# Optimization experiments

Measured on AMD Instinct MI355X. Metric: run time of the kernel, lower is better.

## Reference

```python
import jax, jax.numpy as jnp
import numpy as np

B, S, D, H = 4, 1024, 1024, 16
DK = D // H
NEG = -1e9


def setup_inputs() -> dict:
    key = jax.random.key(0)
    ks = jax.random.split(key, 14)
    sc = 1.0 / np.sqrt(D)
    inp = {
        "query": jax.random.normal(ks[0], (B, S, D), jnp.float32),
        "key": jax.random.normal(ks[1], (B, S, D), jnp.float32),
        "value": jax.random.normal(ks[2], (B, S, D), jnp.float32),
        "mask": jax.random.randint(ks[3], (B, S, S), 0, 2, jnp.int32),
        "group_prob": jax.random.uniform(ks[4], (B, S, S), jnp.float32),
        "Wq": jax.random.normal(ks[5], (D, D), jnp.float32) * sc,
        "bq": jnp.zeros((D,), jnp.float32),
        "Wk": jax.random.normal(ks[6], (D, D), jnp.float32) * sc,
        "bk": jnp.zeros((D,), jnp.float32),
        "Wv": jax.random.normal(ks[7], (D, D), jnp.float32) * sc,
        "bv": jnp.zeros((D,), jnp.float32),
        "Wo": jax.random.normal(ks[8], (D, D), jnp.float32) * sc,
        "bo": jnp.zeros((D,), jnp.float32),
    }
    return inp


def reference(query, key, value, mask, group_prob, Wq, bq, Wk, bk, Wv, bv, Wo, bo):
    # QKV projections, split heads: [B,S,D] -> [B,H,S,DK]
    def proj(x, W, b):
        return (x @ W.T + b).reshape(B, S, H, DK).transpose(0, 2, 1, 3)

    q = proj(query, Wq, bq)
    k = proj(key, Wk, bk)
    v = proj(value, Wv, bv)

    scores = jnp.einsum("bhqd,bhkd->bhqk", q, k) / jnp.sqrt(jnp.float32(DK))

    # group_prob branch: allowed where mask OR diagonal is nonzero
    diag = jnp.eye(S, dtype=jnp.int32)
    allowed = (mask[:, None, :, :] | diag[None, None, :, :]) != 0  # [B,1,S,S]
    scores = jnp.where(allowed, scores, NEG)

    p_attn = jax.nn.softmax(scores, axis=-1)
    p_attn = p_attn * group_prob[:, None, :, :]  # post-softmax group reweighting

    x = jnp.einsum("bhqk,bhkd->bhqd", p_attn, v)
    x = x.transpose(0, 2, 1, 3).reshape(B, S, D)
    return x @ Wo.T + bo
```

## Files before the change

kernel.cpp:

```cpp
#include <hip/hip_runtime.h>
#include <hip/hip_bf16.h>


#define AS1q __attribute__((address_space(1)))
#define AS3q __attribute__((address_space(3)))

typedef __attribute__((ext_vector_type(8))) __bf16 bf16x8;
typedef __attribute__((ext_vector_type(4))) float f32x4;
typedef __attribute__((ext_vector_type(8))) unsigned short u16x8;

#define GSTR 40

__device__ __forceinline__ void gload_lds16(const void* g, void* l) {
  __builtin_amdgcn_global_load_lds((const AS1q void*)g, (AS3q void*)l, 16, 0, 0);
}
__device__ __forceinline__ bf16x8 lds_read8(const unsigned short* p) {
  bf16x8 r;
  __builtin_memcpy(&r, __builtin_assume_aligned(p, 16), 16);
  return r;
}
__device__ __forceinline__ void lds_write8(unsigned short* p, const void* v) {
  __builtin_memcpy(__builtin_assume_aligned(p, 16), v, 16);
}
__device__ __forceinline__ u16x8 cvt8h(const float4 a, const float4 b) {
  const float fv[8] = {a.x, a.y, a.z, a.w, b.x, b.y, b.z, b.w};
  union { u16x8 v; __bf16 e[8]; } hh;
#pragma unroll
  for (int i = 0; i < 8; ++i) hh.e[i] = (__bf16)fv[i];
  return hh.v;
}
__device__ __forceinline__ void cvt8hl(const float4 a, const float4 b, u16x8* hi, u16x8* lo) {
  const float fv[8] = {a.x, a.y, a.z, a.w, b.x, b.y, b.z, b.w};
  union { u16x8 v; __bf16 e[8]; } hh, ll;
#pragma unroll
  for (int i = 0; i < 8; ++i) {
    const __bf16 h = (__bf16)fv[i];
    hh.e[i] = h;
    ll.e[i] = (__bf16)(fv[i] - (float)h);
  }
  *hi = hh.v; *lo = ll.v;
}
__device__ __forceinline__ unsigned short bfbits(float f) {
  const __bf16 h = (__bf16)f;
  unsigned short u; __builtin_memcpy(&u, &h, 2); return u;
}

__global__ __launch_bounds__(256) void k_prep(
    const int* __restrict__ Mask, const float* __restrict__ Gp, float* __restrict__ G2)
{
  const size_t f = (size_t)blockIdx.x * 256 + threadIdx.x;
  const size_t e = f << 2;
  const int k0 = (int)(e & 1023), q = (int)((e >> 10) & 1023);
  const int4 m4 = *(const int4*)(Mask + e);
  const float4 g4 = *(const float4*)(Gp + e);
  float4 r;
  r.x = (m4.x | (q == k0 + 0)) ? g4.x : -1.f;
  r.y = (m4.y | (q == k0 + 1)) ? g4.y : -1.f;
  r.z = (m4.z | (q == k0 + 2)) ? g4.z : -1.f;
  r.w = (m4.w | (q == k0 + 3)) ? g4.w : -1.f;
  *(float4*)(G2 + e) = r;
}

__global__ __launch_bounds__(256) void k_gemm_qkv(
    const float* __restrict__ X0, const float* __restrict__ X1, const float* __restrict__ X2,
    const float* __restrict__ W0, const float* __restrict__ W1, const float* __restrict__ W2,
    const float* __restrict__ B0, const float* __restrict__ B1, const float* __restrict__ B2,
    unsigned short* __restrict__ O0, unsigned short* __restrict__ O1,
    unsigned short* __restrict__ O2)
{
  const int z = blockIdx.z;
  const float* X = (z == 0) ? X0 : (z == 1) ? X1 : X2;
  const float* W = (z == 0) ? W0 : (z == 1) ? W1 : W2;
  const float* Bi = (z == 0) ? B0 : (z == 1) ? B1 : B2;
  unsigned short* O = (z == 0) ? O0 : (z == 1) ? O1 : O2;

  const int bid = blockIdx.x;
  const int swz = (bid & 7) * 64 + (bid >> 3);
  const int n0 = (swz & 15) * 64, m0 = (swz >> 4) * 128;

  __shared__ alignas(16) unsigned short Ah[128 * GSTR];
  __shared__ alignas(16) unsigned short Bh[64 * GSTR];
  const int tid = threadIdx.x, l = tid & 63, w = tid >> 6;
  const int wr = w >> 1, wc = w & 1;

  f32x4 acc[4][2];
#pragma unroll
  for (int i = 0; i < 4; ++i)
#pragma unroll
    for (int j = 0; j < 2; ++j) acc[i][j] = (f32x4){0.f, 0.f, 0.f, 0.f};

  const int arow = tid >> 1, ac0 = (tid & 1) * 16;
  const int brow = tid >> 2, bc0 = (tid & 3) * 8;
  const float* xsrc = X + (size_t)(m0 + arow) * 1024 + ac0;
  const float* wsrc = W + (size_t)(n0 + brow) * 1024 + bc0;

  float4 fx[4], fw[2];
#pragma unroll
  for (int i = 0; i < 4; ++i) fx[i] = *(const float4*)(xsrc + i * 4);
#pragma unroll
  for (int i = 0; i < 2; ++i) fw[i] = *(const float4*)(wsrc + i * 4);

  for (int kt = 0; kt < 32; ++kt) {
    u16x8 xh[2], wh1;
    xh[0] = cvt8h(fx[0], fx[1]);
    xh[1] = cvt8h(fx[2], fx[3]);
    wh1 = cvt8h(fw[0], fw[1]);
    if (kt < 31) {
      const float* nx = xsrc + (kt + 1) * 32;
      const float* nw = wsrc + (kt + 1) * 32;
#pragma unroll
      for (int i = 0; i < 4; ++i) fx[i] = *(const float4*)(nx + i * 4);
#pragma unroll
      for (int i = 0; i < 2; ++i) fw[i] = *(const float4*)(nw + i * 4);
    }
    __syncthreads();
    lds_write8(&Ah[arow * GSTR + ac0], &xh[0]);
    lds_write8(&Ah[arow * GSTR + ac0 + 8], &xh[1]);
    lds_write8(&Bh[brow * GSTR + bc0], &wh1);
    __syncthreads();

    bf16x8 ah[4], bh[2];
#pragma unroll
    for (int mf = 0; mf < 4; ++mf) {
      const int r = wr * 64 + mf * 16 + (l & 15);
      ah[mf] = lds_read8(&Ah[r * GSTR + (l >> 4) * 8]);
    }
#pragma unroll
    for (int nf = 0; nf < 2; ++nf) {
      const int r = wc * 32 + nf * 16 + (l & 15);
      bh[nf] = lds_read8(&Bh[r * GSTR + (l >> 4) * 8]);
    }
#pragma unroll
    for (int mf = 0; mf < 4; ++mf)
#pragma unroll
      for (int nf = 0; nf < 2; ++nf)
        acc[mf][nf] = __builtin_amdgcn_mfma_f32_16x16x32_bf16(ah[mf], bh[nf], acc[mf][nf], 0, 0, 0);
  }

#pragma unroll
  for (int nf = 0; nf < 2; ++nf) {
    const int col = n0 + wc * 32 + nf * 16 + (l & 15);
    const float bias = Bi[col];
#pragma unroll
    for (int mf = 0; mf < 4; ++mf) {
      const int rbase = m0 + wr * 64 + mf * 16 + (l >> 4) * 4;
#pragma unroll
      for (int j = 0; j < 4; ++j)
        O[(size_t)(rbase + j) * 1024 + col] = bfbits(acc[mf][nf][j] + bias);
    }
  }
}

__global__ __launch_bounds__(256) void k_gemm_out(
    const unsigned short* __restrict__ X, const float* __restrict__ W,
    const float* __restrict__ Bi, float* __restrict__ Out)
{
  const int bid = blockIdx.x;
  const int swz = (bid & 7) * 128 + (bid >> 3);
  const int n0 = (swz & 15) * 64, m0 = (swz >> 4) * 64;

  __shared__ alignas(16) unsigned short Ah[64 * GSTR];
  __shared__ alignas(16) unsigned short Bh[64 * GSTR], Bl[64 * GSTR];
  const int tid = threadIdx.x, l = tid & 63, w = tid >> 6;
  const int wr = w >> 1, wc = w & 1;

  f32x4 acc[2][2];
#pragma unroll
  for (int i = 0; i < 2; ++i)
#pragma unroll
    for (int j = 0; j < 2; ++j) acc[i][j] = (f32x4){0.f, 0.f, 0.f, 0.f};

  const int srow = tid >> 2, sc0 = (tid & 3) * 8;
  const unsigned short* xsrc = X + (size_t)(m0 + srow) * 1024 + sc0;
  const float* wsrc = W + (size_t)(n0 + srow) * 1024 + sc0;

  u16x8 xcur = *(const u16x8*)xsrc;
  float4 fw[2];
#pragma unroll
  for (int i = 0; i < 2; ++i) fw[i] = *(const float4*)(wsrc + i * 4);

  for (int kt = 0; kt < 32; ++kt) {
    const u16x8 xstage = xcur;
    u16x8 wh1, wl1;
    cvt8hl(fw[0], fw[1], &wh1, &wl1);
    if (kt < 31) {
      xcur = *(const u16x8*)(xsrc + (kt + 1) * 32);
      const float* nw = wsrc + (kt + 1) * 32;
#pragma unroll
      for (int i = 0; i < 2; ++i) fw[i] = *(const float4*)(nw + i * 4);
    }
    __syncthreads();
    lds_write8(&Ah[srow * GSTR + sc0], &xstage);
    lds_write8(&Bh[srow * GSTR + sc0], &wh1);
    lds_write8(&Bl[srow * GSTR + sc0], &wl1);
    __syncthreads();

    bf16x8 ah[2], bh[2], bl[2];
#pragma unroll
    for (int mf = 0; mf < 2; ++mf) {
      const int r = wr * 32 + mf * 16 + (l & 15);
      ah[mf] = lds_read8(&Ah[r * GSTR + (l >> 4) * 8]);
    }
#pragma unroll
    for (int nf = 0; nf < 2; ++nf) {
      const int r = wc * 32 + nf * 16 + (l & 15);
      bh[nf] = lds_read8(&Bh[r * GSTR + (l >> 4) * 8]);
      bl[nf] = lds_read8(&Bl[r * GSTR + (l >> 4) * 8]);
    }
#pragma unroll
    for (int mf = 0; mf < 2; ++mf)
#pragma unroll
      for (int nf = 0; nf < 2; ++nf) {
        acc[mf][nf] = __builtin_amdgcn_mfma_f32_16x16x32_bf16(ah[mf], bh[nf], acc[mf][nf], 0, 0, 0);
        acc[mf][nf] = __builtin_amdgcn_mfma_f32_16x16x32_bf16(ah[mf], bl[nf], acc[mf][nf], 0, 0, 0);
      }
  }

#pragma unroll
  for (int nf = 0; nf < 2; ++nf) {
    const int col = n0 + wc * 32 + nf * 16 + (l & 15);
    const float bias = Bi[col];
#pragma unroll
    for (int mf = 0; mf < 2; ++mf) {
      const int rbase = m0 + wr * 32 + mf * 16 + (l >> 4) * 4;
#pragma unroll
      for (int j = 0; j < 4; ++j)
        Out[(size_t)(rbase + j) * 1024 + col] = acc[mf][nf][j] + bias;
    }
  }
}

__global__ __launch_bounds__(256) void k_attn(
    const unsigned short* Qh, const unsigned short* __restrict__ Kb,
    const unsigned short* __restrict__ Vb,
    const float* __restrict__ G2, unsigned short* Xo)
{
  const int i = blockIdx.x;
  const int xc = i & 7, kk_ = i >> 3;
  const int h = kk_ & 15, g = kk_ >> 4;
  const int qb = g * 8 + xc;
  const int qt = qb >> 2, b = qb & 3;

  __shared__ alignas(16) unsigned short Kh[2][64 * 64];
  __shared__ alignas(16) unsigned short Vh[64 * 64];
  __shared__ alignas(16) unsigned short Ph[64 * 64];
  const int tid = threadIdx.x, l = tid & 63, w = tid >> 6;

  const unsigned short* kb_ = Kb + (size_t)b * 1048576 + h * 64;
  const unsigned short* vb_ = Vb + (size_t)b * 1048576 + h * 64;

  bf16x8 aq[2];
  {
    const int qrow = qt * 64 + w * 16 + (l & 15);
    const unsigned short* qp_ = Qh + ((size_t)(b * 1024 + qrow)) * 1024 + h * 64;
    aq[0] = lds_read8(qp_ + (l >> 4) * 8);
    aq[1] = lds_read8(qp_ + 32 + (l >> 4) * 8);
  }

  f32x4 accO[4];
#pragma unroll
  for (int nf = 0; nf < 4; ++nf) accO[nf] = (f32x4){0.f, 0.f, 0.f, 0.f};
  float zacc[4] = {0.f, 0.f, 0.f, 0.f};

  const int qloc0 = w * 16 + (l >> 4) * 4;
  const int qg0 = qt * 64 + qloc0;
  const int mcol = l & 15;

  const float* grow[4];
#pragma unroll
  for (int j = 0; j < 4; ++j)
    grow[j] = G2 + (((size_t)(b * 1024 + qg0 + j)) << 10) + mcol;

  const int srcg8 = ((l & 7) ^ (l >> 3)) * 8;
  const int rowl = l >> 3;
  const int kb4 = (tid & 15) * 4, db4 = (tid >> 4) * 4;
  union U4 { unsigned int u[2]; unsigned short s[4]; };
  U4 vr[4];

#pragma unroll
  for (int I = 0; I < 2; ++I)
    gload_lds16(kb_ + (size_t)(I * 32 + w * 8 + rowl) * 1024 + srcg8,
                &Kh[0][I * 2048 + w * 512]);
#pragma unroll
  for (int ii = 0; ii < 4; ++ii)
    __builtin_memcpy(&vr[ii], vb_ + (size_t)(kb4 + ii) * 1024 + db4, 8);

  float gcur[4][4], gnext[4][4];
#pragma unroll
  for (int nf = 0; nf < 4; ++nf)
#pragma unroll
    for (int j = 0; j < 4; ++j) gcur[nf][j] = grow[j][nf * 16];

  int buf = 0;
  for (int kt = 0; kt < 16; ++kt) {
    __syncthreads();

#pragma unroll
    for (int ii = 0; ii < 4; ++ii) {
      const int d = db4 + ii;
      union { unsigned short s[4]; unsigned long long v; } pk;
#pragma unroll
      for (int u = 0; u < 4; ++u) pk.s[u] = vr[u].s[ii];
      const int c = kb4 ^ ((d & 7) << 3);
      __builtin_memcpy(__builtin_assume_aligned(&Vh[d * 64 + c], 8), &pk.v, 8);
    }
    __syncthreads();

    if (kt < 15) {
#pragma unroll
      for (int I = 0; I < 2; ++I)
        gload_lds16(kb_ + (size_t)((kt + 1) * 64 + I * 32 + w * 8 + rowl) * 1024 + srcg8,
                    &Kh[buf ^ 1][I * 2048 + w * 512]);
#pragma unroll
      for (int ii = 0; ii < 4; ++ii)
        __builtin_memcpy(&vr[ii], vb_ + (size_t)((kt + 1) * 64 + kb4 + ii) * 1024 + db4, 8);
#pragma unroll
      for (int nf = 0; nf < 4; ++nf)
#pragma unroll
        for (int j = 0; j < 4; ++j) gnext[nf][j] = grow[j][(kt + 1) * 64 + nf * 16];
    }

#pragma unroll
    for (int nf = 0; nf < 4; ++nf) {
      f32x4 sacc = (f32x4){0.f, 0.f, 0.f, 0.f};
      const int kr = nf * 16 + (l & 15);
#pragma unroll
      for (int ks = 0; ks < 2; ++ks) {
        const int c = (ks * 32 + (l >> 4) * 8) ^ ((kr & 7) << 3);
        sacc = __builtin_amdgcn_mfma_f32_16x16x32_bf16(aq[ks], lds_read8(&Kh[buf][kr * 64 + c]), sacc, 0, 0, 0);
      }
#pragma unroll
      for (int j = 0; j < 4; ++j) {
        const float g2 = gcur[nf][j];
        const float e = (g2 >= 0.f) ? exp2f(fmaf(sacc[j], 0.18033688f, -17.31234049f)) : 0.f;
        zacc[j] += e;
        const int qloc = qloc0 + j;
        Ph[qloc * 64 + ((nf * 16 + mcol) ^ ((qloc & 7) << 3))] = bfbits(e * g2);
      }
    }
    bf16x8 pah[2];
    {
      const int ar = w * 16 + (l & 15);
#pragma unroll
      for (int ks = 0; ks < 2; ++ks) {
        const int c = (ks * 32 + (l >> 4) * 8) ^ ((ar & 7) << 3);
        pah[ks] = lds_read8(&Ph[ar * 64 + c]);
      }
    }
#pragma unroll
    for (int nf = 0; nf < 4; ++nf) {
      const int dr = nf * 16 + (l & 15);
#pragma unroll
      for (int ks = 0; ks < 2; ++ks) {
        const int c = (ks * 32 + (l >> 4) * 8) ^ ((dr & 7) << 3);
        accO[nf] = __builtin_amdgcn_mfma_f32_16x16x32_bf16(pah[ks], lds_read8(&Vh[dr * 64 + c]), accO[nf], 0, 0, 0);
      }
    }
    buf ^= 1;
#pragma unroll
    for (int nf = 0; nf < 4; ++nf)
#pragma unroll
      for (int j = 0; j < 4; ++j) gcur[nf][j] = gnext[nf][j];
  }

#pragma unroll
  for (int j = 0; j < 4; ++j) {
#pragma unroll
    for (int off = 1; off < 16; off <<= 1) zacc[j] += __shfl_xor(zacc[j], off, 64);
  }
  float rz[4];
#pragma unroll
  for (int j = 0; j < 4; ++j) rz[j] = 1.f / zacc[j];

#pragma unroll
  for (int nf = 0; nf < 4; ++nf) {
    const int d = nf * 16 + (l & 15);
#pragma unroll
    for (int j = 0; j < 4; ++j) {
      const int qg = qg0 + j;
      Xo[((size_t)(b * 1024 + qg)) * 1024 + h * 64 + d] = bfbits(accO[nf][j] * rz[j]);
    }
  }
}

extern "C" void kernel_launch(void* const* d_in, const int* in_sizes, int n_in,
                              void* d_out, int out_size, void* d_ws, size_t ws_size,
                              hipStream_t stream) {
  const float* query = (const float*)d_in[0];
  const float* key_in = (const float*)d_in[1];
  const float* value = (const float*)d_in[2];
  const int* mask = (const int*)d_in[3];
  const float* gp = (const float*)d_in[4];
  const float* Wq = (const float*)d_in[5];
  const float* bq = (const float*)d_in[6];
  const float* Wk = (const float*)d_in[7];
  const float* bk = (const float*)d_in[8];
  const float* Wv = (const float*)d_in[9];
  const float* bv = (const float*)d_in[10];
  const float* Wo = (const float*)d_in[11];
  const float* bo = (const float*)d_in[12];
  float* out = (float*)d_out;

  unsigned short* kp = (unsigned short*)d_ws;
  unsigned short* vp = kp + 4194304;
  unsigned short* qp = vp + 4194304;
  unsigned short* xo = qp;
  float* g2 = (float*)(qp + 4194304);

  hipLaunchKernelGGL(k_prep, dim3(4096), dim3(256), 0, stream, mask, gp, g2);
  hipLaunchKernelGGL(k_gemm_qkv, dim3(512, 1, 3), dim3(256), 0, stream,
                     query, key_in, value, Wq, Wk, Wv, bq, bk, bv, qp, kp, vp);
  hipLaunchKernelGGL(k_attn, dim3(1024), dim3(256), 0, stream,
                     qp, kp, vp, g2, xo);
  hipLaunchKernelGGL(k_gemm_out, dim3(1024), dim3(256), 0, stream,
                     xo, Wo, bo, out);
}
```

Baseline: 186.3 us.

## Pre-convert QKV weights to bf16 and double-buffer LDS in QKV GEMM

Adds a separate kernel that converts Wq/Wk/Wv to bf16 once per call, so the QKV GEMM reads half the weight bytes and skips per-tile weight conversion. The QKV GEMM now uses double-buffered LDS tiles with a two-stage register prefetch, which cuts the barriers per k-step from two to one. The cost is an extra launch, extra workspace traffic for the bf16 weight copies, and twice the LDS per block.

```diff
diff --git a/kernel.cpp b/kernel.cpp
--- a/kernel.cpp
+++ b/kernel.cpp
@@ -45,7 +45,7 @@
   unsigned short u; __builtin_memcpy(&u, &h, 2); return u;
 }
 
-__global__ __launch_bounds__(256) void k_prep(
+__global__ __launch_bounds__(256) void k_prep_g2(
     const int* __restrict__ Mask, const float* __restrict__ Gp, float* __restrict__ G2)
 {
   const size_t f = (size_t)blockIdx.x * 256 + threadIdx.x;
@@ -61,16 +61,32 @@
   *(float4*)(G2 + e) = r;
 }
 
+__global__ __launch_bounds__(256) void k_prep_w(
+    const float* __restrict__ Wq, const float* __restrict__ Wk,
+    const float* __restrict__ Wv,
+    unsigned short* __restrict__ Qw, unsigned short* __restrict__ Kw,
+    unsigned short* __restrict__ Vw)
+{
+  const int z = blockIdx.z;
+  const size_t e = ((size_t)blockIdx.x * 256 + threadIdx.x) * 8;
+  const float* S = (z == 0) ? Wq : (z == 1) ? Wk : Wv;
+  unsigned short* D = (z == 0) ? Qw : (z == 1) ? Kw : Vw;
+  const float4 a = *(const float4*)(S + e);
+  const float4 b = *(const float4*)(S + e + 4);
+  *(u16x8*)(D + e) = cvt8h(a, b);
+}
+
 __global__ __launch_bounds__(256) void k_gemm_qkv(
     const float* __restrict__ X0, const float* __restrict__ X1, const float* __restrict__ X2,
-    const float* __restrict__ W0, const float* __restrict__ W1, const float* __restrict__ W2,
+    const unsigned short* __restrict__ W0, const unsigned short* __restrict__ W1,
+    const unsigned short* __restrict__ W2,
     const float* __restrict__ B0, const float* __restrict__ B1, const float* __restrict__ B2,
     unsigned short* __restrict__ O0, unsigned short* __restrict__ O1,
     unsigned short* __restrict__ O2)
 {
   const int z = blockIdx.z;
   const float* X = (z == 0) ? X0 : (z == 1) ? X1 : X2;
-  const float* W = (z == 0) ? W0 : (z == 1) ? W1 : W2;
+  const unsigned short* W = (z == 0) ? W0 : (z == 1) ? W1 : W2;
   const float* Bi = (z == 0) ? B0 : (z == 1) ? B1 : B2;
   unsigned short* O = (z == 0) ? O0 : (z == 1) ? O1 : O2;
 
@@ -78,8 +94,8 @@
   const int swz = (bid & 7) * 64 + (bid >> 3);
   const int n0 = (swz & 15) * 64, m0 = (swz >> 4) * 128;
 
-  __shared__ alignas(16) unsigned short Ah[128 * GSTR];
-  __shared__ alignas(16) unsigned short Bh[64 * GSTR];
+  __shared__ alignas(16) unsigned short Ah[2][128 * GSTR];
+  __shared__ alignas(16) unsigned short Bh[2][64 * GSTR];
   const int tid = threadIdx.x, l = tid & 63, w = tid >> 6;
   const int wr = w >> 1, wc = w & 1;
 
@@ -92,49 +108,55 @@
   const int arow = tid >> 1, ac0 = (tid & 1) * 16;
   const int brow = tid >> 2, bc0 = (tid & 3) * 8;
   const float* xsrc = X + (size_t)(m0 + arow) * 1024 + ac0;
-  const float* wsrc = W + (size_t)(n0 + brow) * 1024 + bc0;
-
-  float4 fx[4], fw[2];
+  const unsigned short* wsrc = W + (size_t)(n0 + brow) * 1024 + bc0;
+
+  float4 fx[4];
+  u16x8 bx;
 #pragma unroll
   for (int i = 0; i < 4; ++i) fx[i] = *(const float4*)(xsrc + i * 4);
-#pragma unroll
-  for (int i = 0; i < 2; ++i) fw[i] = *(const float4*)(wsrc + i * 4);
-
+  bx = *(const u16x8*)(wsrc);
+  {
+    const u16x8 a0 = cvt8h(fx[0], fx[1]), a1 = cvt8h(fx[2], fx[3]);
+    lds_write8(&Ah[0][arow * GSTR + ac0], &a0);
+    lds_write8(&Ah[0][arow * GSTR + ac0 + 8], &a1);
+    lds_write8(&Bh[0][brow * GSTR + bc0], &bx);
+  }
+#pragma unroll
+  for (int i = 0; i < 4; ++i) fx[i] = *(const float4*)(xsrc + 32 + i * 4);
+  bx = *(const u16x8*)(wsrc + 32);
+
+  int buf = 0;
   for (int kt = 0; kt < 32; ++kt) {
-    u16x8 xh[2], wh1;
-    xh[0] = cvt8h(fx[0], fx[1]);
-    xh[1] = cvt8h(fx[2], fx[3]);
-    wh1 = cvt8h(fw[0], fw[1]);
+    __syncthreads();
     if (kt < 31) {
-      const float* nx = xsrc + (kt + 1) * 32;
-      const float* nw = wsrc + (kt + 1) * 32;
-#pragma unroll
-      for (int i = 0; i < 4; ++i) fx[i] = *(const float4*)(nx + i * 4);
-#pragma unroll
-      for (int i = 0; i < 2; ++i) fw[i] = *(const float4*)(nw + i * 4);
-    }
-    __syncthreads();
-    lds_write8(&Ah[arow * GSTR + ac0], &xh[0]);
-    lds_write8(&Ah[arow * GSTR + ac0 + 8], &xh[1]);
-    lds_write8(&Bh[brow * GSTR + bc0], &wh1);
-    __syncthreads();
-
+      const u16x8 a0 = cvt8h(fx[0], fx[1]), a1 = cvt8h(fx[2], fx[3]);
+      lds_write8(&Ah[buf ^ 1][arow * GSTR + ac0], &a0);
+      lds_write8(&Ah[buf ^ 1][arow * GSTR + ac0 + 8], &a1);
+      lds_write8(&Bh[buf ^ 1][brow * GSTR + bc0], &bx);
+      if (kt < 30) {
+        const float* nx = xsrc + (kt + 2) * 32;
+#pragma unroll
+        for (int i = 0; i < 4; ++i) fx[i] = *(const float4*)(nx + i * 4);
+        bx = *(const u16x8*)(wsrc + (kt + 2) * 32);
+      }
+    }
     bf16x8 ah[4], bh[2];
 #pragma unroll
     for (int mf = 0; mf < 4; ++mf) {
       const int r = wr * 64 + mf * 16 + (l & 15);
-      ah[mf] = lds_read8(&Ah[r * GSTR + (l >> 4) * 8]);
+      ah[mf] = lds_read8(&Ah[buf][r * GSTR + (l >> 4) * 8]);
     }
 #pragma unroll
     for (int nf = 0; nf < 2; ++nf) {
       const int r = wc * 32 + nf * 16 + (l & 15);
-      bh[nf] = lds_read8(&Bh[r * GSTR + (l >> 4) * 8]);
+      bh[nf] = lds_read8(&Bh[buf][r * GSTR + (l >> 4) * 8]);
     }
 #pragma unroll
     for (int mf = 0; mf < 4; ++mf)
 #pragma unroll
       for (int nf = 0; nf < 2; ++nf)
         acc[mf][nf] = __builtin_amdgcn_mfma_f32_16x16x32_bf16(ah[mf], bh[nf], acc[mf][nf], 0, 0, 0);
+    buf ^= 1;
   }
 
 #pragma unroll
@@ -406,10 +428,15 @@
   unsigned short* qp = vp + 4194304;
   unsigned short* xo = qp;
   float* g2 = (float*)(qp + 4194304);
-
-  hipLaunchKernelGGL(k_prep, dim3(4096), dim3(256), 0, stream, mask, gp, g2);
+  unsigned short* wq = (unsigned short*)(g2 + 4194304);
+  unsigned short* wk = wq + 1048576;
+  unsigned short* wv = wk + 1048576;
+
+  hipLaunchKernelGGL(k_prep_g2, dim3(4096), dim3(256), 0, stream, mask, gp, g2);
+  hipLaunchKernelGGL(k_prep_w, dim3(512, 1, 3), dim3(256), 0, stream,
+                     Wq, Wk, Wv, wq, wk, wv);
   hipLaunchKernelGGL(k_gemm_qkv, dim3(512, 1, 3), dim3(256), 0, stream,
-                     query, key_in, value, Wq, Wk, Wv, bq, bk, bv, qp, kp, vp);
+                     query, key_in, value, wq, wk, wv, bq, bk, bv, qp, kp, vp);
   hipLaunchKernelGGL(k_attn, dim3(1024), dim3(256), 0, stream,
                      qp, kp, vp, g2, xo);
   hipLaunchKernelGGL(k_gemm_out, dim3(1024), dim3(256), 0, stream,
```

Result: faster. 178.9 us (-4.0%).
